# Kernel optimization log

Hardware: AMD Instinct MI355X
Metric: run time of the kernel (lower is better)

The kernel has to match this reference:

```python
import jax, jax.numpy as jnp
import numpy as np

D_MODEL = 256
EXPERT_DIM = 512
NUM_EXPERTS = 8
TOP_K = 2
SEQ_LEN = 2048
BATCH = 2


def setup_inputs() -> dict:
    key = jax.random.key(0)
    ks = jax.random.split(key, 8)
    s = 0.02
    x = jax.random.normal(ks[0], (SEQ_LEN, BATCH, D_MODEL), dtype=jnp.float32)
    # gate: torch Linear(d_model, num_experts); store as [d, E] so logits = x @ Wg + bg
    Wg = jax.random.normal(ks[1], (D_MODEL, NUM_EXPERTS), dtype=jnp.float32) * s
    bg = jax.random.normal(ks[2], (NUM_EXPERTS,), dtype=jnp.float32) * s
    bias = jnp.zeros((NUM_EXPERTS,), dtype=jnp.float32)  # dynamic routing bias
    # experts: Linear(d, h) -> ReLU -> Linear(h, d), stacked over E
    W1 = jax.random.normal(ks[3], (NUM_EXPERTS, D_MODEL, EXPERT_DIM), dtype=jnp.float32) * s
    b1 = jax.random.normal(ks[4], (NUM_EXPERTS, EXPERT_DIM), dtype=jnp.float32) * s
    W2 = jax.random.normal(ks[5], (NUM_EXPERTS, EXPERT_DIM, D_MODEL), dtype=jnp.float32) * s
    b2 = jax.random.normal(ks[6], (NUM_EXPERTS, D_MODEL), dtype=jnp.float32) * s
    return {"x": x, "Wg": Wg, "bg": bg, "bias": bias, "W1": W1, "b1": b1, "W2": W2, "b2": b2}


def reference(x, Wg, bg, bias, W1, b1, W2, b2):
    # x: [seq, batch, d] -> flatten tokens
    x_flat = x.reshape(-1, D_MODEL)                      # [T, d]
    gate_logits = x_flat @ Wg + bg + bias                # [T, E]
    topk_vals, topk_idx = jax.lax.top_k(gate_logits, TOP_K)   # [T, K]
    # torch code subtracts the row max (topk_vals[:, :1], sorted desc) then softmaxes;
    # jax.nn.softmax is the same stable computation.
    topk_w = jax.nn.softmax(topk_vals, axis=-1)          # [T, K]
    # combine weights over experts: zero for unchosen experts -> exact same math
    # as the masked gather + scatter-add in the original loop.
    combine = (jax.nn.one_hot(topk_idx, NUM_EXPERTS, dtype=x.dtype)
               * topk_w[..., None]).sum(axis=1)          # [T, E]
    h = jax.nn.relu(jnp.einsum('td,edh->teh', x_flat, W1) + b1)   # [T, E, H]
    y = jnp.einsum('teh,ehd->ted', h, W2) + b2                     # [T, E, d]
    out = jnp.einsum('ted,te->td', y, combine)                     # [T, d]
    # dropout is identity in eval mode (p applied only in training)
    return out.reshape(x.shape)
```

## Files before the change

kernel.cpp:

```cpp
#include <hip/hip_runtime.h>
#include <hip/hip_bf16.h>
#include <math.h>

#define D_MODEL 256
#define EXPERT_DIM 512
#define NUM_EXPERTS 8
#define T_TOKENS 4096
#define TM 32
#define XS_LD 264

typedef unsigned short ushort_t;
typedef short short8_t __attribute__((ext_vector_type(8)));
typedef float f32x4 __attribute__((ext_vector_type(4)));

__device__ __forceinline__ ushort_t f2bf(float f) {
    unsigned int u = __float_as_uint(f);
    u += 0x7FFFu + ((u >> 16) & 1u);
    return (ushort_t)(u >> 16);
}

__global__ void zero_counts_kernel(int* __restrict__ counts)
{
    if (threadIdx.x < NUM_EXPERTS) counts[threadIdx.x] = 0;
}

__global__ __launch_bounds__(256) void prep_kernel(
    const float* __restrict__ x, const float* __restrict__ Wg,
    const float* __restrict__ bg, const float* __restrict__ bias,
    const float* __restrict__ W1, const float* __restrict__ W2,
    ushort_t* __restrict__ W1f, ushort_t* __restrict__ W2f,
    int* __restrict__ counts, int* __restrict__ lists,
    float* __restrict__ wts, int* __restrict__ slots)
{
    __shared__ float xs[256][33];
    __shared__ int lcount[NUM_EXPERTS];
    __shared__ int lbase[NUM_EXPERTS];

    const int tid = threadIdx.x;
    if (blockIdx.x < 16) {
        const int tbase = blockIdx.x * 256;
        if (tid < NUM_EXPERTS) lcount[tid] = 0;
        float acc[NUM_EXPERTS];
#pragma unroll
        for (int e = 0; e < NUM_EXPERTS; ++e) acc[e] = 0.f;

        for (int kc = 0; kc < 8; ++kc) {
            __syncthreads();
#pragma unroll
            for (int it = 0; it < 8; ++it) {
                int pos = it * 256 + tid;
                int tl = pos >> 3, c4 = pos & 7;
                float4 v = *(const float4*)(x + (size_t)(tbase + tl) * D_MODEL
                                            + kc * 32 + c4 * 4);
                xs[tl][c4 * 4 + 0] = v.x; xs[tl][c4 * 4 + 1] = v.y;
                xs[tl][c4 * 4 + 2] = v.z; xs[tl][c4 * 4 + 3] = v.w;
            }
            __syncthreads();
            for (int k = 0; k < 32; ++k) {
                float xv = xs[tid][k];
                const float* wr = Wg + (kc * 32 + k) * NUM_EXPERTS;
#pragma unroll
                for (int e = 0; e < NUM_EXPERTS; ++e) acc[e] += xv * wr[e];
            }
        }
        float v0 = -3.0e38f, v1 = -3.0e38f; int i0 = 0, i1 = 0;
#pragma unroll
        for (int e = 0; e < NUM_EXPERTS; ++e) {
            float v = acc[e] + bg[e] + bias[e];
            if (v > v0) { v1 = v0; i1 = i0; v0 = v; i0 = e; }
            else if (v > v1) { v1 = v; i1 = e; }
        }
        float e1 = __expf(v1 - v0);
        float inv = 1.f / (1.f + e1);
        float w0 = inv, w1 = e1 * inv;

        int p0 = atomicAdd(&lcount[i0], 1);
        int p1 = atomicAdd(&lcount[i1], 1);
        __syncthreads();
        if (tid < NUM_EXPERTS) lbase[tid] = atomicAdd(&counts[tid], lcount[tid]);
        __syncthreads();
        int t = tbase + tid;
        int q0 = lbase[i0] + p0;
        int q1 = lbase[i1] + p1;
        lists[i0 * T_TOKENS + q0] = t;  wts[i0 * T_TOKENS + q0] = w0;
        lists[i1 * T_TOKENS + q1] = t;  wts[i1 * T_TOKENS + q1] = w1;
        slots[t * 2 + 0] = i0 * T_TOKENS + q0;
        slots[t * 2 + 1] = i1 * T_TOKENS + q1;
    } else {
        int gid = (blockIdx.x - 16) * 256 + tid;
        bool isW2 = gid >= 131072;
        int idx = isW2 ? gid - 131072 : gid;
        int lane = idx & 63;
        int l15 = lane & 15, quad = lane >> 4;
        int ks = (idx >> 6) & 7;
        ushort_t o[8];
        if (!isW2) {
            int ntile = (idx >> 9) & 31, e = idx >> 14;
            int nn = ntile * 16 + l15;
            int k0 = ks * 32 + quad * 8;
            const float* s = W1 + ((size_t)e * D_MODEL + k0) * EXPERT_DIM + nn;
#pragma unroll
            for (int j = 0; j < 8; ++j) o[j] = f2bf(s[j * EXPERT_DIM]);
            *(int4*)(W1f + (size_t)idx * 8) = *(int4*)o;
        } else {
            int ntile = (idx >> 9) & 15, half = (idx >> 13) & 1, e = idx >> 14;
            int nn = ntile * 16 + l15;
            int k0 = half * 256 + ks * 32 + quad * 8;
            const float* s = W2 + ((size_t)e * EXPERT_DIM + k0) * D_MODEL + nn;
#pragma unroll
            for (int j = 0; j < 8; ++j) o[j] = f2bf(s[j * D_MODEL]);
            *(int4*)(W2f + (size_t)idx * 8) = *(int4*)o;
        }
    }
}

__global__ __launch_bounds__(256) void moe_expert_mfma(
    const float* __restrict__ x,
    const ushort_t* __restrict__ W1f, const float* __restrict__ b1,
    const ushort_t* __restrict__ W2f, const float* __restrict__ b2,
    const int* __restrict__ counts, const int* __restrict__ lists,
    const float* __restrict__ wts, float* __restrict__ ybuf)
{
    const int e = blockIdx.x;
    const int half = blockIdx.y;
    const int n = counts[e];
    const int base = blockIdx.z * TM;
    if (base >= n) return;
    const int m = min(TM, n - base);

    __shared__ ushort_t Xs[TM * XS_LD];
    __shared__ ushort_t Hs[TM * XS_LD];
    __shared__ int   toks[TM];
    __shared__ float wt_s[TM];

    const int tid = threadIdx.x;
    const int lane = tid & 63;
    const int w = tid >> 6;
    const int l15 = lane & 15;
    const int quad = lane >> 4;

    const ushort_t* W1p = W1f + (size_t)(e * 32 + half * 16 + w * 4) * 4096 + lane * 8;
    short8_t bc[4];
#pragma unroll
    for (int nt = 0; nt < 4; ++nt) bc[nt] = *(const short8_t*)(W1p + nt * 4096);

    if (tid < TM) {
        const int* lst = lists + e * T_TOKENS + base;
        const float* wr = wts + e * T_TOKENS + base;
        toks[tid] = (tid < m) ? lst[tid] : -1;
        wt_s[tid] = (tid < m) ? wr[tid] : 0.f;
    }
    __syncthreads();

    for (int c = tid; c < TM * 32; c += 256) {
        int r = c >> 5, c8 = c & 31;
        int tk = toks[r];
        ushort_t o[8];
        if (tk >= 0) {
            const float* src = x + (size_t)tk * D_MODEL + c8 * 8;
            float4 v0 = *(const float4*)src;
            float4 v1 = *(const float4*)(src + 4);
            o[0] = f2bf(v0.x); o[1] = f2bf(v0.y); o[2] = f2bf(v0.z); o[3] = f2bf(v0.w);
            o[4] = f2bf(v1.x); o[5] = f2bf(v1.y); o[6] = f2bf(v1.z); o[7] = f2bf(v1.w);
        } else {
#pragma unroll
            for (int j = 0; j < 8; ++j) o[j] = 0;
        }
        *(int4*)(Xs + r * XS_LD + c8 * 8) = *(int4*)o;
    }
    __syncthreads();

    float b1v[4];
#pragma unroll
    for (int nt = 0; nt < 4; ++nt)
        b1v[nt] = b1[e * EXPERT_DIM + half * 256 + w * 64 + nt * 16 + l15];

    f32x4 acc1[2][4] = {};
    for (int ks = 0; ks < 8; ++ks) {
        short8_t bn[4];
        if (ks < 7) {
#pragma unroll
            for (int nt = 0; nt < 4; ++nt)
                bn[nt] = *(const short8_t*)(W1p + nt * 4096 + (ks + 1) * 512);
        }
        short8_t a0 = *(const short8_t*)(Xs + l15 * XS_LD + ks * 32 + quad * 8);
        short8_t a1 = *(const short8_t*)(Xs + (16 + l15) * XS_LD + ks * 32 + quad * 8);
#pragma unroll
        for (int nt = 0; nt < 4; ++nt) {
            acc1[0][nt] = __builtin_amdgcn_mfma_f32_16x16x32_bf16(a0, bc[nt], acc1[0][nt], 0, 0, 0);
            acc1[1][nt] = __builtin_amdgcn_mfma_f32_16x16x32_bf16(a1, bc[nt], acc1[1][nt], 0, 0, 0);
        }
        if (ks < 7) {
#pragma unroll
            for (int nt = 0; nt < 4; ++nt) bc[nt] = bn[nt];
        }
    }

    const ushort_t* W2p = W2f + (size_t)((e * 2 + half) * 16 + w * 4) * 4096 + lane * 8;
    short8_t bc2[4];
#pragma unroll
    for (int nt = 0; nt < 4; ++nt) bc2[nt] = *(const short8_t*)(W2p + nt * 4096);
    float b2v[4];
#pragma unroll
    for (int nt = 0; nt < 4; ++nt)
        b2v[nt] = half ? b2[e * D_MODEL + w * 64 + nt * 16 + l15] : 0.f;

#pragma unroll
    for (int mt = 0; mt < 2; ++mt)
#pragma unroll
        for (int nt = 0; nt < 4; ++nt)
#pragma unroll
            for (int r = 0; r < 4; ++r) {
                int row = mt * 16 + quad * 4 + r;
                int col = w * 64 + nt * 16 + l15;
                float h = fmaxf(acc1[mt][nt][r] + b1v[nt], 0.f);
                Hs[row * XS_LD + col] = f2bf(h);
            }
    __syncthreads();

    f32x4 acc2[2][4] = {};
    for (int ks = 0; ks < 8; ++ks) {
        short8_t bn2[4];
        if (ks < 7) {
#pragma unroll
            for (int nt = 0; nt < 4; ++nt)
                bn2[nt] = *(const short8_t*)(W2p + nt * 4096 + (ks + 1) * 512);
        }
        short8_t a0 = *(const short8_t*)(Hs + l15 * XS_LD + ks * 32 + quad * 8);
        short8_t a1 = *(const short8_t*)(Hs + (16 + l15) * XS_LD + ks * 32 + quad * 8);
#pragma unroll
        for (int nt = 0; nt < 4; ++nt) {
            acc2[0][nt] = __builtin_amdgcn_mfma_f32_16x16x32_bf16(a0, bc2[nt], acc2[0][nt], 0, 0, 0);
            acc2[1][nt] = __builtin_amdgcn_mfma_f32_16x16x32_bf16(a1, bc2[nt], acc2[1][nt], 0, 0, 0);
        }
        if (ks < 7) {
#pragma unroll
            for (int nt = 0; nt < 4; ++nt) bc2[nt] = bn2[nt];
        }
    }

    float* yrow = ybuf + ((size_t)(half * NUM_EXPERTS + e) * T_TOKENS + base) * D_MODEL;
#pragma unroll
    for (int mt = 0; mt < 2; ++mt)
#pragma unroll
        for (int nt = 0; nt < 4; ++nt)
#pragma unroll
            for (int r = 0; r < 4; ++r) {
                int row = mt * 16 + quad * 4 + r;
                if (row < m) {
                    int col = w * 64 + nt * 16 + l15;
                    yrow[(size_t)row * D_MODEL + col] =
                        wt_s[row] * (acc2[mt][nt][r] + b2v[nt]);
                }
            }
}

__global__ __launch_bounds__(256) void combine_kernel(
    const int* __restrict__ slots, const float* __restrict__ ybuf,
    float* __restrict__ out)
{
    int gid = blockIdx.x * 256 + threadIdx.x;
    int t = gid >> 6, lane = gid & 63;
    int s0 = slots[t * 2 + 0];
    int s1 = slots[t * 2 + 1];
    const size_t H = (size_t)NUM_EXPERTS * T_TOKENS * D_MODEL;
    float4 a = ((const float4*)(ybuf + (size_t)s0 * D_MODEL))[lane];
    float4 b = ((const float4*)(ybuf + (size_t)s0 * D_MODEL + H))[lane];
    float4 c = ((const float4*)(ybuf + (size_t)s1 * D_MODEL))[lane];
    float4 d = ((const float4*)(ybuf + (size_t)s1 * D_MODEL + H))[lane];
    float4 r;
    r.x = a.x + b.x + c.x + d.x;
    r.y = a.y + b.y + c.y + d.y;
    r.z = a.z + b.z + c.z + d.z;
    r.w = a.w + b.w + c.w + d.w;
    ((float4*)(out + (size_t)t * D_MODEL))[lane] = r;
}

extern "C" void kernel_launch(void* const* d_in, const int* in_sizes, int n_in,
                              void* d_out, int out_size, void* d_ws, size_t ws_size,
                              hipStream_t stream)
{
    const float* x    = (const float*)d_in[0];
    const float* Wg   = (const float*)d_in[1];
    const float* bg   = (const float*)d_in[2];
    const float* bias = (const float*)d_in[3];
    const float* W1   = (const float*)d_in[4];
    const float* b1   = (const float*)d_in[5];
    const float* W2   = (const float*)d_in[6];
    const float* b2   = (const float*)d_in[7];
    float* out = (float*)d_out;

    char* ws = (char*)d_ws;
    int*      counts = (int*)ws;
    int*      lists  = (int*)(ws + 256);
    float*    wts    = (float*)(ws + 256 + 131072);
    int*      slots  = (int*)(ws + 256 + 262144);
    ushort_t* W1f    = (ushort_t*)(ws + 256 + 294912);
    ushort_t* W2f    = (ushort_t*)(ws + 256 + 294912 + 2097152);
    float*    ybuf   = (float*)(ws + 256 + 294912 + 4194304);

    zero_counts_kernel<<<1, 64, 0, stream>>>(counts);

    prep_kernel<<<1040, 256, 0, stream>>>(
        x, Wg, bg, bias, W1, W2, W1f, W2f, counts, lists, wts, slots);

    moe_expert_mfma<<<dim3(NUM_EXPERTS, 2, T_TOKENS / TM), 256, 0, stream>>>(
        x, W1f, b1, W2f, b2, counts, lists, wts, ybuf);

    combine_kernel<<<T_TOKENS * 64 / 256, 256, 0, stream>>>(slots, ybuf, out);
}
```

Measured before the change: 117.2 us.

## Double expert token tile, preload weight fragments, and precast x to bf16 in prep

Expert tile grows from 32 to 64 tokens, and each wave now loads all W1/W2 B-fragments into registers up front, so every weight load is reused across four M-tiles instead of two. The prep kernel writes a bf16 copy of x that the expert kernel gathers directly, dropping the per-expert fp32 load and convert. Gating now uses 128-token blocks with K split across two thread halves to spread the work over more blocks. The cost is heavy register pressure (64 short8 fragments plus 32 accumulators under launch_bounds 256,2), more padding waste on partial tiles, and fewer expert blocks in flight.

```diff
diff --git a/kernel.cpp b/kernel.cpp
--- a/kernel.cpp
+++ b/kernel.cpp
@@ -6,7 +6,7 @@
 #define EXPERT_DIM 512
 #define NUM_EXPERTS 8
 #define T_TOKENS 4096
-#define TM 32
+#define TM 64
 #define XS_LD 264
 
 typedef unsigned short ushort_t;
@@ -29,16 +29,20 @@
     const float* __restrict__ bg, const float* __restrict__ bias,
     const float* __restrict__ W1, const float* __restrict__ W2,
     ushort_t* __restrict__ W1f, ushort_t* __restrict__ W2f,
+    ushort_t* __restrict__ xb,
     int* __restrict__ counts, int* __restrict__ lists,
     float* __restrict__ wts, int* __restrict__ slots)
 {
-    __shared__ float xs[256][33];
+    __shared__ float xs[128][33];
+    __shared__ float accbuf[128][9];
     __shared__ int lcount[NUM_EXPERTS];
     __shared__ int lbase[NUM_EXPERTS];
 
     const int tid = threadIdx.x;
-    if (blockIdx.x < 16) {
-        const int tbase = blockIdx.x * 256;
+    if (blockIdx.x < 32) {
+        const int tbase = blockIdx.x * 128;
+        const int tl = tid & 127;
+        const int kh = tid >> 7;
         if (tid < NUM_EXPERTS) lcount[tid] = 0;
         float acc[NUM_EXPERTS];
 #pragma unroll
@@ -47,47 +51,66 @@
         for (int kc = 0; kc < 8; ++kc) {
             __syncthreads();
 #pragma unroll
-            for (int it = 0; it < 8; ++it) {
+            for (int it = 0; it < 4; ++it) {
                 int pos = it * 256 + tid;
-                int tl = pos >> 3, c4 = pos & 7;
-                float4 v = *(const float4*)(x + (size_t)(tbase + tl) * D_MODEL
-                                            + kc * 32 + c4 * 4);
-                xs[tl][c4 * 4 + 0] = v.x; xs[tl][c4 * 4 + 1] = v.y;
-                xs[tl][c4 * 4 + 2] = v.z; xs[tl][c4 * 4 + 3] = v.w;
+                int r = pos >> 3, c4 = pos & 7;
+                const float* src = x + (size_t)(tbase + r) * D_MODEL + kc * 32 + c4 * 4;
+                float4 v = *(const float4*)src;
+                xs[r][c4 * 4 + 0] = v.x; xs[r][c4 * 4 + 1] = v.y;
+                xs[r][c4 * 4 + 2] = v.z; xs[r][c4 * 4 + 3] = v.w;
+                ushort4 o;
+                o.x = f2bf(v.x); o.y = f2bf(v.y); o.z = f2bf(v.z); o.w = f2bf(v.w);
+                *(ushort4*)&xb[(size_t)(tbase + r) * D_MODEL + kc * 32 + c4 * 4] = o;
             }
             __syncthreads();
-            for (int k = 0; k < 32; ++k) {
-                float xv = xs[tid][k];
+            for (int k = kh * 16; k < kh * 16 + 16; ++k) {
+                float xv = xs[tl][k];
                 const float* wr = Wg + (kc * 32 + k) * NUM_EXPERTS;
 #pragma unroll
                 for (int e = 0; e < NUM_EXPERTS; ++e) acc[e] += xv * wr[e];
             }
         }
-        float v0 = -3.0e38f, v1 = -3.0e38f; int i0 = 0, i1 = 0;
-#pragma unroll
-        for (int e = 0; e < NUM_EXPERTS; ++e) {
-            float v = acc[e] + bg[e] + bias[e];
-            if (v > v0) { v1 = v0; i1 = i0; v0 = v; i0 = e; }
-            else if (v > v1) { v1 = v; i1 = e; }
-        }
-        float e1 = __expf(v1 - v0);
-        float inv = 1.f / (1.f + e1);
-        float w0 = inv, w1 = e1 * inv;
-
-        int p0 = atomicAdd(&lcount[i0], 1);
-        int p1 = atomicAdd(&lcount[i1], 1);
+        __syncthreads();
+        if (kh == 1) {
+#pragma unroll
+            for (int e = 0; e < NUM_EXPERTS; ++e) accbuf[tl][e] = acc[e];
+        }
+        __syncthreads();
+        if (kh == 0) {
+            float v0 = -3.0e38f, v1 = -3.0e38f; int i0 = 0, i1 = 0;
+#pragma unroll
+            for (int e = 0; e < NUM_EXPERTS; ++e) {
+                float v = acc[e] + accbuf[tl][e] + bg[e] + bias[e];
+                if (v > v0) { v1 = v0; i1 = i0; v0 = v; i0 = e; }
+                else if (v > v1) { v1 = v; i1 = e; }
+            }
+            float e1 = __expf(v1 - v0);
+            float inv = 1.f / (1.f + e1);
+            float w0 = inv, w1 = e1 * inv;
+
+            int p0 = atomicAdd(&lcount[i0], 1);
+            int p1 = atomicAdd(&lcount[i1], 1);
+            accbuf[tl][0] = w0; accbuf[tl][1] = w1;
+            accbuf[tl][2] = __int_as_float(i0 * T_TOKENS + p0);
+            accbuf[tl][3] = __int_as_float(i1 * T_TOKENS + p1);
+        }
         __syncthreads();
         if (tid < NUM_EXPERTS) lbase[tid] = atomicAdd(&counts[tid], lcount[tid]);
         __syncthreads();
-        int t = tbase + tid;
-        int q0 = lbase[i0] + p0;
-        int q1 = lbase[i1] + p1;
-        lists[i0 * T_TOKENS + q0] = t;  wts[i0 * T_TOKENS + q0] = w0;
-        lists[i1 * T_TOKENS + q1] = t;  wts[i1 * T_TOKENS + q1] = w1;
-        slots[t * 2 + 0] = i0 * T_TOKENS + q0;
-        slots[t * 2 + 1] = i1 * T_TOKENS + q1;
+        if (kh == 0) {
+            int t = tbase + tl;
+            int s0 = __float_as_int(accbuf[tl][2]);
+            int s1 = __float_as_int(accbuf[tl][3]);
+            int q0 = s0 % T_TOKENS + lbase[s0 / T_TOKENS];
+            int q1 = s1 % T_TOKENS + lbase[s1 / T_TOKENS];
+            int i0 = s0 / T_TOKENS, i1 = s1 / T_TOKENS;
+            lists[i0 * T_TOKENS + q0] = t;  wts[i0 * T_TOKENS + q0] = accbuf[tl][0];
+            lists[i1 * T_TOKENS + q1] = t;  wts[i1 * T_TOKENS + q1] = accbuf[tl][1];
+            slots[t * 2 + 0] = i0 * T_TOKENS + q0;
+            slots[t * 2 + 1] = i1 * T_TOKENS + q1;
+        }
     } else {
-        int gid = (blockIdx.x - 16) * 256 + tid;
+        int gid = (blockIdx.x - 32) * 256 + tid;
         bool isW2 = gid >= 131072;
         int idx = isW2 ? gid - 131072 : gid;
         int lane = idx & 63;
@@ -114,8 +137,8 @@
     }
 }
 
-__global__ __launch_bounds__(256) void moe_expert_mfma(
-    const float* __restrict__ x,
+__global__ __launch_bounds__(256, 2) void moe_expert_mfma(
+    const ushort_t* __restrict__ xb,
     const ushort_t* __restrict__ W1f, const float* __restrict__ b1,
     const ushort_t* __restrict__ W2f, const float* __restrict__ b2,
     const int* __restrict__ counts, const int* __restrict__ lists,
@@ -140,9 +163,12 @@
     const int quad = lane >> 4;
 
     const ushort_t* W1p = W1f + (size_t)(e * 32 + half * 16 + w * 4) * 4096 + lane * 8;
-    short8_t bc[4];
-#pragma unroll
-    for (int nt = 0; nt < 4; ++nt) bc[nt] = *(const short8_t*)(W1p + nt * 4096);
+    short8_t b1f[4][8];
+#pragma unroll
+    for (int nt = 0; nt < 4; ++nt)
+#pragma unroll
+        for (int ks = 0; ks < 8; ++ks)
+            b1f[nt][ks] = *(const short8_t*)(W1p + nt * 4096 + ks * 512);
 
     if (tid < TM) {
         const int* lst = lists + e * T_TOKENS + base;
@@ -155,18 +181,9 @@
     for (int c = tid; c < TM * 32; c += 256) {
         int r = c >> 5, c8 = c & 31;
         int tk = toks[r];
-        ushort_t o[8];
-        if (tk >= 0) {
-            const float* src = x + (size_t)tk * D_MODEL + c8 * 8;
-            float4 v0 = *(const float4*)src;
-            float4 v1 = *(const float4*)(src + 4);
-            o[0] = f2bf(v0.x); o[1] = f2bf(v0.y); o[2] = f2bf(v0.z); o[3] = f2bf(v0.w);
-            o[4] = f2bf(v1.x); o[5] = f2bf(v1.y); o[6] = f2bf(v1.z); o[7] = f2bf(v1.w);
-        } else {
-#pragma unroll
-            for (int j = 0; j < 8; ++j) o[j] = 0;
-        }
-        *(int4*)(Xs + r * XS_LD + c8 * 8) = *(int4*)o;
+        int4 v = make_int4(0, 0, 0, 0);
+        if (tk >= 0) v = *(const int4*)(xb + (size_t)tk * D_MODEL + c8 * 8);
+        *(int4*)(Xs + r * XS_LD + c8 * 8) = v;
     }
     __syncthreads();
 
@@ -175,38 +192,34 @@
     for (int nt = 0; nt < 4; ++nt)
         b1v[nt] = b1[e * EXPERT_DIM + half * 256 + w * 64 + nt * 16 + l15];
 
-    f32x4 acc1[2][4] = {};
+    f32x4 acc1[4][4] = {};
     for (int ks = 0; ks < 8; ++ks) {
-        short8_t bn[4];
-        if (ks < 7) {
+        short8_t a[4];
+#pragma unroll
+        for (int mt = 0; mt < 4; ++mt)
+            a[mt] = *(const short8_t*)(Xs + (mt * 16 + l15) * XS_LD + ks * 32 + quad * 8);
+#pragma unroll
+        for (int mt = 0; mt < 4; ++mt)
 #pragma unroll
             for (int nt = 0; nt < 4; ++nt)
-                bn[nt] = *(const short8_t*)(W1p + nt * 4096 + (ks + 1) * 512);
-        }
-        short8_t a0 = *(const short8_t*)(Xs + l15 * XS_LD + ks * 32 + quad * 8);
-        short8_t a1 = *(const short8_t*)(Xs + (16 + l15) * XS_LD + ks * 32 + quad * 8);
-#pragma unroll
-        for (int nt = 0; nt < 4; ++nt) {
-            acc1[0][nt] = __builtin_amdgcn_mfma_f32_16x16x32_bf16(a0, bc[nt], acc1[0][nt], 0, 0, 0);
-            acc1[1][nt] = __builtin_amdgcn_mfma_f32_16x16x32_bf16(a1, bc[nt], acc1[1][nt], 0, 0, 0);
-        }
-        if (ks < 7) {
-#pragma unroll
-            for (int nt = 0; nt < 4; ++nt) bc[nt] = bn[nt];
-        }
+                acc1[mt][nt] = __builtin_amdgcn_mfma_f32_16x16x32_bf16(
+                    a[mt], b1f[nt][ks], acc1[mt][nt], 0, 0, 0);
     }
 
     const ushort_t* W2p = W2f + (size_t)((e * 2 + half) * 16 + w * 4) * 4096 + lane * 8;
-    short8_t bc2[4];
-#pragma unroll
-    for (int nt = 0; nt < 4; ++nt) bc2[nt] = *(const short8_t*)(W2p + nt * 4096);
+    short8_t b2f[4][8];
+#pragma unroll
+    for (int nt = 0; nt < 4; ++nt)
+#pragma unroll
+        for (int ks = 0; ks < 8; ++ks)
+            b2f[nt][ks] = *(const short8_t*)(W2p + nt * 4096 + ks * 512);
     float b2v[4];
 #pragma unroll
     for (int nt = 0; nt < 4; ++nt)
         b2v[nt] = half ? b2[e * D_MODEL + w * 64 + nt * 16 + l15] : 0.f;
 
 #pragma unroll
-    for (int mt = 0; mt < 2; ++mt)
+    for (int mt = 0; mt < 4; ++mt)
 #pragma unroll
         for (int nt = 0; nt < 4; ++nt)
 #pragma unroll
@@ -218,30 +231,23 @@
             }
     __syncthreads();
 
-    f32x4 acc2[2][4] = {};
+    f32x4 acc2[4][4] = {};
     for (int ks = 0; ks < 8; ++ks) {
-        short8_t bn2[4];
-        if (ks < 7) {
+        short8_t a[4];
+#pragma unroll
+        for (int mt = 0; mt < 4; ++mt)
+            a[mt] = *(const short8_t*)(Hs + (mt * 16 + l15) * XS_LD + ks * 32 + quad * 8);
+#pragma unroll
+        for (int mt = 0; mt < 4; ++mt)
 #pragma unroll
             for (int nt = 0; nt < 4; ++nt)
-                bn2[nt] = *(const short8_t*)(W2p + nt * 4096 + (ks + 1) * 512);
-        }
-        short8_t a0 = *(const short8_t*)(Hs + l15 * XS_LD + ks * 32 + quad * 8);
-        short8_t a1 = *(const short8_t*)(Hs + (16 + l15) * XS_LD + ks * 32 + quad * 8);
-#pragma unroll
-        for (int nt = 0; nt < 4; ++nt) {
-            acc2[0][nt] = __builtin_amdgcn_mfma_f32_16x16x32_bf16(a0, bc2[nt], acc2[0][nt], 0, 0, 0);
-            acc2[1][nt] = __builtin_amdgcn_mfma_f32_16x16x32_bf16(a1, bc2[nt], acc2[1][nt], 0, 0, 0);
-        }
-        if (ks < 7) {
-#pragma unroll
-            for (int nt = 0; nt < 4; ++nt) bc2[nt] = bn2[nt];
-        }
+                acc2[mt][nt] = __builtin_amdgcn_mfma_f32_16x16x32_bf16(
+                    a[mt], b2f[nt][ks], acc2[mt][nt], 0, 0, 0);
     }
 
     float* yrow = ybuf + ((size_t)(half * NUM_EXPERTS + e) * T_TOKENS + base) * D_MODEL;
 #pragma unroll
-    for (int mt = 0; mt < 2; ++mt)
+    for (int mt = 0; mt < 4; ++mt)
 #pragma unroll
         for (int nt = 0; nt < 4; ++nt)
 #pragma unroll
@@ -293,19 +299,20 @@
     char* ws = (char*)d_ws;
     int*      counts = (int*)ws;
     int*      lists  = (int*)(ws + 256);
-    float*    wts    = (float*)(ws + 256 + 131072);
-    int*      slots  = (int*)(ws + 256 + 262144);
-    ushort_t* W1f    = (ushort_t*)(ws + 256 + 294912);
-    ushort_t* W2f    = (ushort_t*)(ws + 256 + 294912 + 2097152);
-    float*    ybuf   = (float*)(ws + 256 + 294912 + 4194304);
+    float*    wts    = (float*)(ws + 131328);
+    int*      slots  = (int*)(ws + 262400);
+    ushort_t* xb     = (ushort_t*)(ws + 524288);
+    ushort_t* W1f    = (ushort_t*)(ws + 2621440);
+    ushort_t* W2f    = (ushort_t*)(ws + 4718592);
+    float*    ybuf   = (float*)(ws + 6815744);
 
     zero_counts_kernel<<<1, 64, 0, stream>>>(counts);
 
-    prep_kernel<<<1040, 256, 0, stream>>>(
-        x, Wg, bg, bias, W1, W2, W1f, W2f, counts, lists, wts, slots);
+    prep_kernel<<<1056, 256, 0, stream>>>(
+        x, Wg, bg, bias, W1, W2, W1f, W2f, xb, counts, lists, wts, slots);
 
     moe_expert_mfma<<<dim3(NUM_EXPERTS, 2, T_TOKENS / TM), 256, 0, stream>>>(
-        x, W1f, b1, W2f, b2, counts, lists, wts, ybuf);
+        xb, W1f, b1, W2f, b2, counts, lists, wts, ybuf);
 
     combine_kernel<<<T_TOKENS * 64 / 256, 256, 0, stream>>>(slots, ybuf, out);
 }
```

Result: no change. 115.9 us (-1.0%).
